# Kernel tuning notes

Hardware: AMD Instinct MI355X
Metric: run time of the kernel (lower is better)

The kernel has to match this reference:

```python
import jax, jax.numpy as jnp
import numpy as np

N_NODES = 100000
N_EDGES = 1600000
N_GRAPHS = 1000
HID = 64
NEG_SLOPE = 0.2


def _glorot(key, shape):
    fan_in, fan_out = shape[0], shape[-1]
    lim = float(np.sqrt(6.0 / (fan_in + fan_out)))
    return jax.random.uniform(key, shape, jnp.float32, -lim, lim)


def setup_inputs() -> dict:
    key = jax.random.key(0)
    ks = jax.random.split(key, 20)
    x = jax.random.normal(ks[0], (N_NODES, 1), jnp.float32)
    edge_index = jax.random.randint(ks[1], (2, N_EDGES), 0, N_NODES, jnp.int64)
    batch = jnp.sort(jax.random.randint(ks[2], (N_NODES,), 0, N_GRAPHS, jnp.int64))
    inp = {"x": x, "edge_index": edge_index, "batch": batch}
    # GATv2Conv layer 1 (in=3 -> out=HID, 1 head)
    inp["Wl1"] = _glorot(ks[3], (3, HID)); inp["bl1"] = jnp.zeros((HID,), jnp.float32)
    inp["Wr1"] = _glorot(ks[4], (3, HID)); inp["br1"] = jnp.zeros((HID,), jnp.float32)
    inp["a1"] = _glorot(ks[5], (HID, 1))[:, 0]; inp["b1"] = jnp.zeros((HID,), jnp.float32)
    # GATv2Conv layer 2 (HID -> HID)
    inp["Wl2"] = _glorot(ks[6], (HID, HID)); inp["bl2"] = jnp.zeros((HID,), jnp.float32)
    inp["Wr2"] = _glorot(ks[7], (HID, HID)); inp["br2"] = jnp.zeros((HID,), jnp.float32)
    inp["a2"] = _glorot(ks[8], (HID, 1))[:, 0]; inp["b2"] = jnp.zeros((HID,), jnp.float32)
    # lin2 (HID -> 2)
    inp["W3"] = _glorot(ks[9], (HID, 2)); inp["b3"] = jnp.zeros((2,), jnp.float32)
    return inp


def gatv2_layer(x, src, dst, Wl, bl, Wr, br, a, b):
    """GATv2Conv, 1 head, add_self_loops=True, negative_slope=0.2."""
    n = x.shape[0]
    xl = x @ Wl + bl  # source-side transform [N, C]
    xr = x @ Wr + br  # target-side transform [N, C]
    loops = jnp.arange(n, dtype=src.dtype)
    s = jnp.concatenate([src, loops])
    d = jnp.concatenate([dst, loops])
    # per-edge attention logit: a^T LeakyReLU(xl[j] + xr[i])
    e = jax.nn.leaky_relu(xl[s] + xr[d], NEG_SLOPE) @ a  # [E+N]
    # segment softmax over incoming edges of each dst node
    m = jax.ops.segment_max(e, d, num_segments=n)
    ex = jnp.exp(e - m[d])
    denom = jax.ops.segment_sum(ex, d, num_segments=n)
    alpha = ex / denom[d]
    out = jax.ops.segment_sum(alpha[:, None] * xl[s], d, num_segments=n)
    return out + b


def reference(x, edge_index, batch, Wl1, bl1, Wr1, br1, a1, b1,
              Wl2, bl2, Wr2, br2, a2, b2, W3, b3):
    n = x.shape[0]
    src, dst = edge_index[0], edge_index[1]
    ones = jnp.ones((src.shape[0],), jnp.float32)
    deg_in = jax.ops.segment_sum(ones, dst, num_segments=n)   # bincount(dst)
    deg_out = jax.ops.segment_sum(ones, src, num_segments=n)  # bincount(src)
    h = jnp.concatenate([x, deg_in[:, None], deg_out[:, None]], axis=1)  # [N,3]
    h = gatv2_layer(h, src, dst, Wl1, bl1, Wr1, br1, a1, b1)
    h = jnp.tanh(h)
    h = gatv2_layer(h, src, dst, Wl2, bl2, Wr2, br2, a2, b2)
    # global_max_pool over graphs
    g = jax.ops.segment_max(h, batch, num_segments=N_GRAPHS)  # [G, HID]
    return g @ W3 + b3  # [G, 2]
```

## Files before the change

### kernel.cpp

```cpp
#include <hip/hip_runtime.h>
#include <hip/hip_bf16.h>
#include <hip/hip_fp16.h>

#define HID 64
#define NEG_SLOPE 0.2f
#define BLK_E 4096
#define EDGE_CAP 6144
#define NDB 16

typedef _Float16 f16x2 __attribute__((ext_vector_type(2)));
typedef _Float16 f16x8 __attribute__((ext_vector_type(8)));
typedef float f32x4 __attribute__((ext_vector_type(4)));


__global__ void k_hist2(const int* __restrict__ src, const int* __restrict__ dst,
                        int* __restrict__ histS, int* __restrict__ histD,
                        int E, int NB, int NBLK) {
    __shared__ int hs[512], hd[512];
    int t = threadIdx.x, blk = blockIdx.x;
    for (int b = t; b < NB; b += 1024) { hs[b] = 0; hd[b] = 0; }
    __syncthreads();
    int base = blk * BLK_E;
    #pragma unroll
    for (int k = 0; k < BLK_E / 1024; ++k) {
        int i = base + k * 1024 + t;
        if (i < E) {
            atomicAdd(&hs[src[i] >> 8], 1);
            atomicAdd(&hd[dst[i] >> 8], 1);
        }
    }
    __syncthreads();
    for (int b = t; b < NB; b += 1024) {
        histS[b * NBLK + blk] = hs[b];
        histD[b * NBLK + blk] = hd[b];
    }
}

__global__ void k_binscan(int* __restrict__ histS, int* __restrict__ histD,
                          int* __restrict__ totS, int* __restrict__ totD,
                          int NB, int NBLK) {
    __shared__ int s[512];
    int b = blockIdx.x;
    int* hist = histS; int* tot = totS;
    if (b >= NB) { b -= NB; hist = histD; tot = totD; }
    int t = threadIdx.x;
    int v = (t < NBLK) ? hist[b * NBLK + t] : 0;
    s[t] = v;
    __syncthreads();
    for (int o = 1; o < 512; o <<= 1) {
        int u = (t >= o) ? s[t - o] : 0;
        __syncthreads();
        s[t] += u;
        __syncthreads();
    }
    if (t < NBLK) hist[b * NBLK + t] = s[t] - v;
    if (t == 511) tot[b] = s[511];
}

__global__ void k_binoffset(const int* __restrict__ totS, const int* __restrict__ totD,
                            int* __restrict__ bsS, int* __restrict__ bsD,
                            int NB, int E, int* __restrict__ row_off, int N) {
    __shared__ int s[512];
    int t = threadIdx.x;
    int v = (t < NB) ? totS[t] : 0;
    s[t] = v; __syncthreads();
    for (int o = 1; o < 512; o <<= 1) {
        int u = (t >= o) ? s[t - o] : 0;
        __syncthreads(); s[t] += u; __syncthreads();
    }
    if (t < NB) bsS[t] = s[t] - v;
    if (t == 0) bsS[NB] = E;
    __syncthreads();
    v = (t < NB) ? totD[t] : 0;
    s[t] = v; __syncthreads();
    for (int o = 1; o < 512; o <<= 1) {
        int u = (t >= o) ? s[t - o] : 0;
        __syncthreads(); s[t] += u; __syncthreads();
    }
    if (t < NB) bsD[t] = s[t] - v;
    if (t == 0) { bsD[NB] = E; row_off[N] = E; }
}

__global__ void k_scatter_bins(const int* __restrict__ src, const int* __restrict__ dst,
                               const int* __restrict__ histS, const int* __restrict__ histD,
                               const int* __restrict__ bsS, const int* __restrict__ bsD,
                               unsigned* __restrict__ packS, unsigned* __restrict__ packD,
                               int E, int NB, int NBLK) {
    __shared__ int baseS[512], baseD[512];
    int t = threadIdx.x, blk = blockIdx.x;
    for (int b = t; b < NB; b += 1024) {
        baseS[b] = bsS[b] + histS[b * NBLK + blk];
        baseD[b] = bsD[b] + histD[b * NBLK + blk];
    }
    __syncthreads();
    int base = blk * BLK_E;
    #pragma unroll
    for (int k = 0; k < BLK_E / 1024; ++k) {
        int i = base + k * 1024 + t;
        if (i < E) {
            int sv = src[i], dv = dst[i];
            int pD = atomicAdd(&baseD[dv >> 8], 1);
            packD[pD] = ((unsigned)(dv & 255) << 24) | (unsigned)sv;
            int pS = atomicAdd(&baseS[sv >> 8], 1);
            packS[pS] = (unsigned)(sv & 255);
        }
    }
}

__global__ void k_csr_bin_fused(const unsigned* __restrict__ packD, const int* __restrict__ bsD,
                                const unsigned* __restrict__ packS, const int* __restrict__ bsS,
                                int* __restrict__ row_off, float* __restrict__ deg_in,
                                int* __restrict__ csr_src,
                                const float* __restrict__ x,
                                const float* __restrict__ Wl, const float* __restrict__ bl,
                                const float* __restrict__ Wr, const float* __restrict__ br,
                                __half* __restrict__ A, __half* __restrict__ B, int N) {
    __shared__ int cnt[256], off[256], cur[256], cntS[256];
    __shared__ unsigned eb[EDGE_CAP];
    int b = blockIdx.x, t = threadIdx.x;
    int lo = bsD[b], hi = bsD[b + 1], ne = hi - lo;
    bool fits = (ne <= EDGE_CAP);
    if (t < 256) { cnt[t] = 0; cntS[t] = 0; }
    __syncthreads();
    for (int i = t; i < ne; i += 1024) {
        unsigned v = packD[lo + i];
        if (fits) eb[i] = v;
        atomicAdd(&cnt[v >> 24], 1);
    }
    int loS = bsS[b], hiS = bsS[b + 1];
    for (int i = loS + t; i < hiS; i += 1024) atomicAdd(&cntS[packS[i] & 255], 1);
    __syncthreads();
    if (t < 256) off[t] = cnt[t];
    __syncthreads();
    for (int o = 1; o < 256; o <<= 1) {
        int u = 0;
        if (t < 256 && t >= o) u = off[t - o];
        __syncthreads();
        if (t < 256) off[t] += u;
        __syncthreads();
    }
    if (t < 256) {
        int ex = off[t] - cnt[t];
        cur[t] = lo + ex;
        int node = b * 256 + t;
        if (node < N) {
            row_off[node] = lo + ex;
            deg_in[node] = (float)cnt[t];
        }
    }
    __syncthreads();
    for (int i = t; i < ne; i += 1024) {
        unsigned v = fits ? eb[i] : packD[lo + i];
        int pos = atomicAdd(&cur[v >> 24], 1);
        csr_src[pos] = (int)(v & 0xFFFFFFu);
    }
    int nd = b * 256 + (t >> 2);
    if (nd < N) {
        float h0 = x[nd];
        float h1 = (float)cnt[t >> 2];
        float h2 = (float)cntS[t >> 2];
        int c0 = (t & 3) * 16;
        unsigned ua[4], ub[4];
        #pragma unroll
        for (int p = 0; p < 2; ++p) {
            #pragma unroll
            for (int q = 0; q < 4; ++q) {
                int c = c0 + p * 8 + q * 2;
                float a0 = h0 * Wl[c]     + h1 * Wl[64 + c]     + h2 * Wl[128 + c]     + bl[c];
                float a1 = h0 * Wl[c + 1] + h1 * Wl[64 + c + 1] + h2 * Wl[128 + c + 1] + bl[c + 1];
                float b0 = h0 * Wr[c]     + h1 * Wr[64 + c]     + h2 * Wr[128 + c]     + br[c];
                float b1 = h0 * Wr[c + 1] + h1 * Wr[64 + c + 1] + h2 * Wr[128 + c + 1] + br[c + 1];
                f16x2 pa; pa.x = (_Float16)a0; pa.y = (_Float16)a1;
                f16x2 pb; pb.x = (_Float16)b0; pb.y = (_Float16)b1;
                ua[q] = __builtin_bit_cast(unsigned, pa);
                ub[q] = __builtin_bit_cast(unsigned, pb);
            }
            uint4 sa = make_uint4(ua[0], ua[1], ua[2], ua[3]);
            uint4 sb = make_uint4(ub[0], ub[1], ub[2], ub[3]);
            ((uint4*)A)[(size_t)nd * 8 + (t & 3) * 2 + p] = sa;
            ((uint4*)B)[(size_t)nd * 8 + (t & 3) * 2 + p] = sb;
        }
    }
}


__global__ void k_deghist(const float* __restrict__ deg_in, int* __restrict__ dhist, int N) {
    __shared__ int h[64];
    int t = threadIdx.x, b = blockIdx.x;
    if (t < 64) h[t] = 0;
    __syncthreads();
    int chunk = (N + NDB - 1) / NDB;
    int lo = b * chunk, hi = lo + chunk; if (hi > N) hi = N;
    for (int i = lo + t; i < hi; i += 1024) {
        int dg = (int)deg_in[i]; if (dg > 63) dg = 63;
        atomicAdd(&h[dg], 1);
    }
    __syncthreads();
    if (t < 64) dhist[t * NDB + b] = h[t];
}

__global__ void k_degscan(int* __restrict__ dhist) {
    __shared__ int s[1024];
    int t = threadIdx.x;
    int v = dhist[t];
    s[t] = v; __syncthreads();
    for (int o = 1; o < 1024; o <<= 1) {
        int u = (t >= o) ? s[t - o] : 0;
        __syncthreads(); s[t] += u; __syncthreads();
    }
    dhist[t] = s[t] - v;
}

__global__ void k_degscatter(const float* __restrict__ deg_in, const int* __restrict__ dhist,
                             int* __restrict__ perm, int N) {
    __shared__ int cur[64];
    int t = threadIdx.x, b = blockIdx.x;
    if (t < 64) cur[t] = dhist[t * NDB + b];
    __syncthreads();
    int chunk = (N + NDB - 1) / NDB;
    int lo = b * chunk, hi = lo + chunk; if (hi > N) hi = N;
    for (int i = lo + t; i < hi; i += 1024) {
        int dg = (int)deg_in[i]; if (dg > 63) dg = 63;
        int p = atomicAdd(&cur[dg], 1);
        perm[p] = i;
    }
}


struct H4 { f16x2 h[4]; };

__device__ __forceinline__ f16x2 bch2(unsigned u) {
    return __builtin_bit_cast(f16x2, u);
}

__device__ __forceinline__ H4 ld4(const uint4* __restrict__ T, size_t idx) {
    uint4 r = T[idx];
    H4 o;
    o.h[0] = bch2(r.x); o.h[1] = bch2(r.y); o.h[2] = bch2(r.z); o.h[3] = bch2(r.w);
    return o;
}

__device__ __forceinline__ float logit8(const H4& a, const H4& x,
                                        const float* __restrict__ awf, f16x2 ns2) {
    float t = 0.0f;
    #pragma unroll
    for (int j = 0; j < 4; ++j) {
        f16x2 s = a.h[j] + x.h[j];
        f16x2 l = __builtin_elementwise_max(s, ns2 * s);
        t = fmaf((float)l.x, awf[2 * j], t);
        t = fmaf((float)l.y, awf[2 * j + 1], t);
    }
    return t;
}

__device__ __forceinline__ void accum8(float* __restrict__ acc, const H4& a, float w) {
    #pragma unroll
    for (int j = 0; j < 4; ++j) {
        acc[2 * j]     = fmaf((float)a.h[j].x, w, acc[2 * j]);
        acc[2 * j + 1] = fmaf((float)a.h[j].y, w, acc[2 * j + 1]);
    }
}

template <typename OUT, bool TANH>
__global__ void k_gat_fused(const int* __restrict__ csr_src, const int* __restrict__ row_off,
                            const int* __restrict__ perm,
                            const __half* __restrict__ Ah, const __half* __restrict__ Bh,
                            const float* __restrict__ aw, const float* __restrict__ bias,
                            OUT* __restrict__ out, int N) {
    int tid = blockIdx.x * blockDim.x + threadIdx.x;
    int r = tid >> 3;
    int gl = threadIdx.x & 7;
    if (r >= N) return;
    int d = perm[N - 1 - r];

    const uint4* A16 = (const uint4*)Ah;
    const uint4* B16 = (const uint4*)Bh;
    f16x2 ns2;
    ns2.x = (_Float16)NEG_SLOPE; ns2.y = (_Float16)NEG_SLOPE;

    float awf[8], bw[8];
    {
        const float4* a4 = (const float4*)aw;
        const float4* b4 = (const float4*)bias;
        #pragma unroll
        for (int j = 0; j < 2; ++j) {
            float4 v = a4[gl * 2 + j];
            awf[4 * j] = v.x; awf[4 * j + 1] = v.y; awf[4 * j + 2] = v.z; awf[4 * j + 3] = v.w;
            float4 u = b4[gl * 2 + j];
            bw[4 * j] = u.x; bw[4 * j + 1] = u.y; bw[4 * j + 2] = u.z; bw[4 * j + 3] = u.w;
        }
    }

    size_t rowbase = (size_t)d * 8 + gl;
    H4 xh = ld4(B16, rowbase);
    H4 as = ld4(A16, rowbase);

    float t = logit8(as, xh, awf, ns2);
    t += __shfl_xor(t, 1); t += __shfl_xor(t, 2); t += __shfl_xor(t, 4);
    float m = t, denom = 1.0f;
    float acc[8];
    #pragma unroll
    for (int j = 0; j < 4; ++j) {
        acc[2 * j] = (float)as.h[j].x;
        acc[2 * j + 1] = (float)as.h[j].y;
    }

    int lo = row_off[d], hi = row_off[d + 1];
    int k = lo;
    for (; k + 3 < hi; k += 4) {
        int s0 = csr_src[k], s1 = csr_src[k + 1], s2 = csr_src[k + 2], s3 = csr_src[k + 3];
        H4 a0 = ld4(A16, (size_t)s0 * 8 + gl);
        H4 a1 = ld4(A16, (size_t)s1 * 8 + gl);
        H4 a2 = ld4(A16, (size_t)s2 * 8 + gl);
        H4 a3 = ld4(A16, (size_t)s3 * 8 + gl);
        float t0 = logit8(a0, xh, awf, ns2);
        float t1 = logit8(a1, xh, awf, ns2);
        float t2 = logit8(a2, xh, awf, ns2);
        float t3 = logit8(a3, xh, awf, ns2);
        t0 += __shfl_xor(t0, 1); t1 += __shfl_xor(t1, 1);
        t2 += __shfl_xor(t2, 1); t3 += __shfl_xor(t3, 1);
        t0 += __shfl_xor(t0, 2); t1 += __shfl_xor(t1, 2);
        t2 += __shfl_xor(t2, 2); t3 += __shfl_xor(t3, 2);
        t0 += __shfl_xor(t0, 4); t1 += __shfl_xor(t1, 4);
        t2 += __shfl_xor(t2, 4); t3 += __shfl_xor(t3, 4);
        float mx = fmaxf(fmaxf(t0, t1), fmaxf(t2, t3));
        if (mx > m) {
            float sc = __expf(m - mx);
            denom *= sc;
            #pragma unroll
            for (int j = 0; j < 8; ++j) acc[j] *= sc;
            m = mx;
        }
        float w0 = __expf(t0 - m), w1 = __expf(t1 - m);
        float w2 = __expf(t2 - m), w3 = __expf(t3 - m);
        denom += (w0 + w1) + (w2 + w3);
        accum8(acc, a0, w0);
        accum8(acc, a1, w1);
        accum8(acc, a2, w2);
        accum8(acc, a3, w3);
    }
    for (; k < hi; ++k) {
        int s0 = csr_src[k];
        H4 a0 = ld4(A16, (size_t)s0 * 8 + gl);
        float t0 = logit8(a0, xh, awf, ns2);
        t0 += __shfl_xor(t0, 1); t0 += __shfl_xor(t0, 2); t0 += __shfl_xor(t0, 4);
        if (t0 > m) {
            float sc = __expf(m - t0);
            denom *= sc;
            #pragma unroll
            for (int j = 0; j < 8; ++j) acc[j] *= sc;
            m = t0;
        }
        float w0 = __expf(t0 - m);
        denom += w0;
        accum8(acc, a0, w0);
    }

    float inv = 1.0f / denom;
    float v[8];
    #pragma unroll
    for (int j = 0; j < 8; ++j) {
        v[j] = acc[j] * inv + bw[j];
        if (TANH) v[j] = tanhf(v[j]);
    }
    if constexpr (sizeof(OUT) == 2) {
        unsigned u[4];
        #pragma unroll
        for (int j = 0; j < 4; ++j) {
            f16x2 p; p.x = (_Float16)v[2 * j]; p.y = (_Float16)v[2 * j + 1];
            u[j] = __builtin_bit_cast(unsigned, p);
        }
        ((uint4*)out)[(size_t)d * 8 + gl] = make_uint4(u[0], u[1], u[2], u[3]);
    } else {
        float4* o4 = (float4*)out;
        o4[(size_t)d * 16 + gl * 2]     = make_float4(v[0], v[1], v[2], v[3]);
        o4[(size_t)d * 16 + gl * 2 + 1] = make_float4(v[4], v[5], v[6], v[7]);
    }
}


__global__ void k_wprep(const float* __restrict__ Wl, const float* __restrict__ Wr,
                        __half* __restrict__ Wtl, __half* __restrict__ Wtr) {
    int t = blockIdx.x * blockDim.x + threadIdx.x;
    if (t < 4096) {
        int c = t & 63, k = t >> 6;
        Wtl[(size_t)c * 64 + k] = __float2half(Wl[k * 64 + c]);
        Wtr[(size_t)c * 64 + k] = __float2half(Wr[k * 64 + c]);
    }
}

__global__ __launch_bounds__(256) void k_xfrm2_mfma(
        const __half* __restrict__ H,
        const __half* __restrict__ Wtl, const __half* __restrict__ Wtr,
        const float* __restrict__ bl, const float* __restrict__ br,
        __half* __restrict__ A, __half* __restrict__ B, int N) {
    int wid = threadIdx.x >> 6;
    int lane = threadIdx.x & 63;
    int n0 = (blockIdx.x * 4 + wid) * 16;
    if (n0 >= N) return;
    int row = lane & 15, kg = lane >> 4;
    int nrow = n0 + row; if (nrow >= N) nrow = N - 1;

    const uint4* Hp = (const uint4*)(H + (size_t)nrow * HID + kg * 8);
    f16x8 af0 = __builtin_bit_cast(f16x8, Hp[0]);
    f16x8 af1 = __builtin_bit_cast(f16x8, Hp[4]);

    #pragma unroll
    for (int tb = 0; tb < 2; ++tb) {
        const __half* Wt = tb ? Wtr : Wtl;
        const float* bb  = tb ? br : bl;
        __half* OT       = tb ? B : A;
        #pragma unroll
        for (int ct = 0; ct < 4; ++ct) {
            int c = ct * 16 + row;
            const uint4* Wp = (const uint4*)(Wt + (size_t)c * HID + kg * 8);
            f16x8 bf0 = __builtin_bit_cast(f16x8, Wp[0]);
            f16x8 bf1 = __builtin_bit_cast(f16x8, Wp[4]);
            f32x4 acc = {0.f, 0.f, 0.f, 0.f};
            acc = __builtin_amdgcn_mfma_f32_16x16x32_f16(af0, bf0, acc, 0, 0, 0);
            acc = __builtin_amdgcn_mfma_f32_16x16x32_f16(af1, bf1, acc, 0, 0, 0);
            float bias = bb[c];
            #pragma unroll
            for (int r = 0; r < 4; ++r) {
                int node = n0 + kg * 4 + r;
                if (node < N) OT[(size_t)node * HID + c] = __float2half(acc[r] + bias);
            }
        }
    }
}

__global__ void k_pool_final(const float* __restrict__ C, const float* __restrict__ b2,
                             const int* __restrict__ batch,
                             const float* __restrict__ W3, const float* __restrict__ b3,
                             float* __restrict__ out, int N, int G) {
    int w = (int)((blockIdx.x * (size_t)blockDim.x + threadIdx.x) >> 6);
    int lane = threadIdx.x & 63;
    if (w >= G) return;
    int lo = 0, hi = N;
    while (lo < hi) { int mid = (lo + hi) >> 1; if (batch[mid] < w) lo = mid + 1; else hi = mid; }
    int s0 = lo;
    hi = N;
    while (lo < hi) { int mid = (lo + hi) >> 1; if (batch[mid] < w + 1) lo = mid + 1; else hi = mid; }
    int e0 = lo;

    float acc = -INFINITY;
    int i = s0;
    for (; i + 3 < e0; i += 4) {
        float v0 = C[(size_t)i * HID + lane];
        float v1 = C[(size_t)(i + 1) * HID + lane];
        float v2 = C[(size_t)(i + 2) * HID + lane];
        float v3 = C[(size_t)(i + 3) * HID + lane];
        acc = fmaxf(acc, fmaxf(fmaxf(v0, v1), fmaxf(v2, v3)));
    }
    for (; i < e0; ++i) acc = fmaxf(acc, C[(size_t)i * HID + lane]);
    float v = acc + b2[lane];

    float p0 = v * W3[lane * 2];
    float p1 = v * W3[lane * 2 + 1];
    #pragma unroll
    for (int o = 32; o; o >>= 1) { p0 += __shfl_xor(p0, o); p1 += __shfl_xor(p1, o); }
    if (lane == 0) {
        out[(size_t)w * 2]     = p0 + b3[0];
        out[(size_t)w * 2 + 1] = p1 + b3[1];
    }
}

extern "C" void kernel_launch(void* const* d_in, const int* in_sizes, int n_in,
                              void* d_out, int out_size, void* d_ws, size_t ws_size,
                              hipStream_t stream) {
    const float* x     = (const float*)d_in[0];
    const int*   ei    = (const int*)d_in[1];
    const int*   batch = (const int*)d_in[2];
    const float* Wl1 = (const float*)d_in[3];
    const float* bl1 = (const float*)d_in[4];
    const float* Wr1 = (const float*)d_in[5];
    const float* br1 = (const float*)d_in[6];
    const float* a1  = (const float*)d_in[7];
    const float* b1  = (const float*)d_in[8];
    const float* Wl2 = (const float*)d_in[9];
    const float* bl2 = (const float*)d_in[10];
    const float* Wr2 = (const float*)d_in[11];
    const float* br2 = (const float*)d_in[12];
    const float* a2  = (const float*)d_in[13];
    const float* b2  = (const float*)d_in[14];
    const float* W3  = (const float*)d_in[15];
    const float* b3  = (const float*)d_in[16];

    const int N = in_sizes[0];
    const int E = in_sizes[1] / 2;
    const int G = out_size / 2;
    const int NB = (N + 255) >> 8;
    const int NBLK = (E + BLK_E - 1) / BLK_E;

    float* ws = (float*)d_ws;
    size_t off = 0;
    float*  C  = ws + off; off += (size_t)N * HID;
    __half* Ah = (__half*)(ws + off); off += (size_t)N * HID / 2;
    __half* Bh = (__half*)(ws + off); off += (size_t)N * HID / 2;
    int*   row_off = (int*)(ws + off); off += N + 1;
    int*   csr_src = (int*)(ws + off); off += E;
    float* deg_in  = ws + off; off += N;
    int*   perm    = (int*)(ws + off); off += N;
    int*   dhist   = (int*)(ws + off); off += 1024;
    int*   bsS  = (int*)(ws + off); off += NB + 1;
    int*   bsD  = (int*)(ws + off); off += NB + 1;
    int*   totS = (int*)(ws + off); off += NB;
    int*   totD = (int*)(ws + off); off += NB;
    off = (off + 3) & ~(size_t)3;
    __half* Wtl = (__half*)(ws + off); off += 2048;
    __half* Wtr = (__half*)(ws + off); off += 2048;

    unsigned* packD = (unsigned*)C;
    unsigned* packS = packD + E;
    int* histS = (int*)(packS + E);
    int* histD = histS + (size_t)NB * NBLK;
    __half* Chalf = (__half*)C;

    const int* src  = ei;
    const int* dstp = ei + E;

    const int BT = 256;
    dim3 blk(BT);
    int grid_g8 = (int)(((size_t)N * 8 + BT - 1) / BT);
    int grid_mf = (N + 63) / 64;

    k_hist2<<<NBLK, 1024, 0, stream>>>(src, dstp, histS, histD, E, NB, NBLK);
    k_binscan<<<2 * NB, 512, 0, stream>>>(histS, histD, totS, totD, NB, NBLK);
    k_binoffset<<<1, 512, 0, stream>>>(totS, totD, bsS, bsD, NB, E, row_off, N);
    k_scatter_bins<<<NBLK, 1024, 0, stream>>>(src, dstp, histS, histD, bsS, bsD,
                                              packS, packD, E, NB, NBLK);
    k_csr_bin_fused<<<NB, 1024, 0, stream>>>(packD, bsD, packS, bsS, row_off, deg_in,
                                             csr_src, x, Wl1, bl1, Wr1, br1, Ah, Bh, N);

    k_deghist<<<NDB, 1024, 0, stream>>>(deg_in, dhist, N);
    k_degscan<<<1, 1024, 0, stream>>>(dhist);
    k_degscatter<<<NDB, 1024, 0, stream>>>(deg_in, dhist, perm, N);
    k_wprep<<<16, 256, 0, stream>>>(Wl2, Wr2, Wtl, Wtr);

    k_gat_fused<__half, true><<<grid_g8, blk, 0, stream>>>(csr_src, row_off, perm,
                                                           Ah, Bh, a1, b1, Chalf, N);

    k_xfrm2_mfma<<<grid_mf, 256, 0, stream>>>(Chalf, Wtl, Wtr, bl2, br2, Ah, Bh, N);
    k_gat_fused<float, false><<<grid_g8, blk, 0, stream>>>(csr_src, row_off, perm,
                                                           Ah, Bh, a2, b2, C, N);

    k_pool_final<<<(G * 64 + BT - 1) / BT, blk, 0, stream>>>(C, b2, batch, W3, b3,
                                                             (float*)d_out, N, G);
}
```

Before: 203.7 us.

## Split each node's edge list across two 8-lane groups and store layer-2 output in fp16

The fused GAT kernel now uses 16 lanes per destination node. Two 8-lane subgroups each process half of the incoming edges with an online softmax, then combine their max, denominator and accumulators through cross-lane shuffles. The aim is more parallelism and memory-level concurrency for high-degree nodes, at the cost of twice the threads and an extra merge step. Separately, the layer-2 output is now written as fp16 and the pooling kernel reads fp16, which halves that write/read traffic but lowers output precision.

```diff
diff --git a/kernel.cpp b/kernel.cpp
--- a/kernel.cpp
+++ b/kernel.cpp
@@ -268,7 +268,8 @@
                             const float* __restrict__ aw, const float* __restrict__ bias,
                             OUT* __restrict__ out, int N) {
     int tid = blockIdx.x * blockDim.x + threadIdx.x;
-    int r = tid >> 3;
+    int r = tid >> 4;
+    int sub = (threadIdx.x >> 3) & 1;
     int gl = threadIdx.x & 7;
     if (r >= N) return;
     int d = perm[N - 1 - r];
@@ -293,21 +294,27 @@
 
     size_t rowbase = (size_t)d * 8 + gl;
     H4 xh = ld4(B16, rowbase);
-    H4 as = ld4(A16, rowbase);
-
-    float t = logit8(as, xh, awf, ns2);
-    t += __shfl_xor(t, 1); t += __shfl_xor(t, 2); t += __shfl_xor(t, 4);
-    float m = t, denom = 1.0f;
-    float acc[8];
-    #pragma unroll
-    for (int j = 0; j < 4; ++j) {
-        acc[2 * j] = (float)as.h[j].x;
-        acc[2 * j + 1] = (float)as.h[j].y;
+
+    float m = -1e30f, denom = 0.0f;
+    float acc[8] = {0, 0, 0, 0, 0, 0, 0, 0};
+
+    if (sub == 0) {
+        H4 as = ld4(A16, rowbase);
+        float t = logit8(as, xh, awf, ns2);
+        t += __shfl_xor(t, 1); t += __shfl_xor(t, 2); t += __shfl_xor(t, 4);
+        m = t; denom = 1.0f;
+        #pragma unroll
+        for (int j = 0; j < 4; ++j) {
+            acc[2 * j] = (float)as.h[j].x;
+            acc[2 * j + 1] = (float)as.h[j].y;
+        }
     }
 
     int lo = row_off[d], hi = row_off[d + 1];
-    int k = lo;
-    for (; k + 3 < hi; k += 4) {
+    int len = hi - lo, half = (len + 1) >> 1;
+    int k   = sub ? lo + half : lo;
+    int khi = sub ? hi : lo + half;
+    for (; k + 3 < khi; k += 4) {
         int s0 = csr_src[k], s1 = csr_src[k + 1], s2 = csr_src[k + 2], s3 = csr_src[k + 3];
         H4 a0 = ld4(A16, (size_t)s0 * 8 + gl);
         H4 a1 = ld4(A16, (size_t)s1 * 8 + gl);
@@ -339,7 +346,7 @@
         accum8(acc, a2, w2);
         accum8(acc, a3, w3);
     }
-    for (; k < hi; ++k) {
+    for (; k < khi; ++k) {
         int s0 = csr_src[k];
         H4 a0 = ld4(A16, (size_t)s0 * 8 + gl);
         float t0 = logit8(a0, xh, awf, ns2);
@@ -356,6 +363,20 @@
         accum8(acc, a0, w0);
     }
 
+    {
+        float mo = __shfl_xor(m, 8);
+        float no = __shfl_xor(denom, 8);
+        float M = fmaxf(m, mo);
+        float s0 = __expf(m - M);
+        float s1 = __expf(mo - M);
+        denom = denom * s0 + no * s1;
+        #pragma unroll
+        for (int j = 0; j < 8; ++j) {
+            float ao = __shfl_xor(acc[j], 8);
+            acc[j] = acc[j] * s0 + ao * s1;
+        }
+    }
+
     float inv = 1.0f / denom;
     float v[8];
     #pragma unroll
@@ -363,18 +384,20 @@
         v[j] = acc[j] * inv + bw[j];
         if (TANH) v[j] = tanhf(v[j]);
     }
-    if constexpr (sizeof(OUT) == 2) {
-        unsigned u[4];
-        #pragma unroll
-        for (int j = 0; j < 4; ++j) {
-            f16x2 p; p.x = (_Float16)v[2 * j]; p.y = (_Float16)v[2 * j + 1];
-            u[j] = __builtin_bit_cast(unsigned, p);
-        }
-        ((uint4*)out)[(size_t)d * 8 + gl] = make_uint4(u[0], u[1], u[2], u[3]);
-    } else {
-        float4* o4 = (float4*)out;
-        o4[(size_t)d * 16 + gl * 2]     = make_float4(v[0], v[1], v[2], v[3]);
-        o4[(size_t)d * 16 + gl * 2 + 1] = make_float4(v[4], v[5], v[6], v[7]);
+    if (sub == 0) {
+        if constexpr (sizeof(OUT) == 2) {
+            unsigned u[4];
+            #pragma unroll
+            for (int j = 0; j < 4; ++j) {
+                f16x2 p; p.x = (_Float16)v[2 * j]; p.y = (_Float16)v[2 * j + 1];
+                u[j] = __builtin_bit_cast(unsigned, p);
+            }
+            ((uint4*)out)[(size_t)d * 8 + gl] = make_uint4(u[0], u[1], u[2], u[3]);
+        } else {
+            float4* o4 = (float4*)out;
+            o4[(size_t)d * 16 + gl * 2]     = make_float4(v[0], v[1], v[2], v[3]);
+            o4[(size_t)d * 16 + gl * 2 + 1] = make_float4(v[4], v[5], v[6], v[7]);
+        }
     }
 }
 
@@ -429,7 +452,7 @@
     }
 }
 
-__global__ void k_pool_final(const float* __restrict__ C, const float* __restrict__ b2,
+__global__ void k_pool_final(const __half* __restrict__ C, const float* __restrict__ b2,
                              const int* __restrict__ batch,
                              const float* __restrict__ W3, const float* __restrict__ b3,
                              float* __restrict__ out, int N, int G) {
@@ -446,13 +469,13 @@
     float acc = -INFINITY;
     int i = s0;
     for (; i + 3 < e0; i += 4) {
-        float v0 = C[(size_t)i * HID + lane];
-        float v1 = C[(size_t)(i + 1) * HID + lane];
-        float v2 = C[(size_t)(i + 2) * HID + lane];
-        float v3 = C[(size_t)(i + 3) * HID + lane];
+        float v0 = __half2float(C[(size_t)i * HID + lane]);
+        float v1 = __half2float(C[(size_t)(i + 1) * HID + lane]);
+        float v2 = __half2float(C[(size_t)(i + 2) * HID + lane]);
+        float v3 = __half2float(C[(size_t)(i + 3) * HID + lane]);
         acc = fmaxf(acc, fmaxf(fmaxf(v0, v1), fmaxf(v2, v3)));
     }
-    for (; i < e0; ++i) acc = fmaxf(acc, C[(size_t)i * HID + lane]);
+    for (; i < e0; ++i) acc = fmaxf(acc, __half2float(C[(size_t)i * HID + lane]));
     float v = acc + b2[lane];
 
     float p0 = v * W3[lane * 2];
@@ -521,8 +544,8 @@
 
     const int BT = 256;
     dim3 blk(BT);
-    int grid_g8 = (int)(((size_t)N * 8 + BT - 1) / BT);
-    int grid_mf = (N + 63) / 64;
+    int grid_g16 = (int)(((size_t)N * 16 + BT - 1) / BT);
+    int grid_mf  = (N + 63) / 64;
 
     k_hist2<<<NBLK, 1024, 0, stream>>>(src, dstp, histS, histD, E, NB, NBLK);
     k_binscan<<<2 * NB, 512, 0, stream>>>(histS, histD, totS, totD, NB, NBLK);
@@ -537,13 +560,13 @@
     k_degscatter<<<NDB, 1024, 0, stream>>>(deg_in, dhist, perm, N);
     k_wprep<<<16, 256, 0, stream>>>(Wl2, Wr2, Wtl, Wtr);
 
-    k_gat_fused<__half, true><<<grid_g8, blk, 0, stream>>>(csr_src, row_off, perm,
-                                                           Ah, Bh, a1, b1, Chalf, N);
+    k_gat_fused<__half, true><<<grid_g16, blk, 0, stream>>>(csr_src, row_off, perm,
+                                                            Ah, Bh, a1, b1, Chalf, N);
 
     k_xfrm2_mfma<<<grid_mf, 256, 0, stream>>>(Chalf, Wtl, Wtr, bl2, br2, Ah, Bh, N);
-    k_gat_fused<float, false><<<grid_g8, blk, 0, stream>>>(csr_src, row_off, perm,
-                                                           Ah, Bh, a2, b2, C, N);
-
-    k_pool_final<<<(G * 64 + BT - 1) / BT, blk, 0, stream>>>(C, b2, batch, W3, b3,
+    k_gat_fused<__half, false><<<grid_g16, blk, 0, stream>>>(csr_src, row_off, perm,
+                                                             Ah, Bh, a2, b2, Chalf, N);
+
+    k_pool_final<<<(G * 64 + BT - 1) / BT, blk, 0, stream>>>(Chalf, b2, batch, W3, b3,
                                                              (float*)d_out, N, G);
 }
```

Measured after the change: 217.8 us. +6.9%, slower.
